# Kernel optimization log

Hardware: AMD Instinct MI355X
Metric: run time of the kernel (lower is better)

## Reference

```python
import jax, jax.numpy as jnp
import numpy as np

B, S, H, A, O = 512, 64, 1024, 1024, 1024
ATT = 64  # attention logit width (== encoder seq len)


def setup_inputs() -> dict:
    key = jax.random.key(0)
    ks = jax.random.split(key, 14)
    s = lambda *sh: 1.0 / np.sqrt(sh[-1])
    return {
        "encoder_outputs": jax.random.normal(ks[0], (B, S, A), jnp.float32),
        "hidden": jax.random.normal(ks[1], (1, B, H), jnp.float32),
        "max_length": 128,
        # attention: Linear(H+O -> 64)
        "Wa": jax.random.normal(ks[2], (ATT, H + O), jnp.float32) * s(H + O),
        "ba": jnp.zeros((ATT,), jnp.float32),
        # attention_combine: Linear(A+O -> H)
        "Wc": jax.random.normal(ks[3], (H, A + O), jnp.float32) * s(A + O),
        "bc": jnp.zeros((H,), jnp.float32),
        # GRU (1 layer): weight_ih [3H,H], weight_hh [3H,H]
        "W_ih": jax.random.normal(ks[4], (3 * H, H), jnp.float32) * s(H),
        "W_hh": jax.random.normal(ks[5], (3 * H, H), jnp.float32) * s(H),
        "b_ih": jnp.zeros((3 * H,), jnp.float32),
        "b_hh": jnp.zeros((3 * H,), jnp.float32),
        # fc_out: Linear(H -> O)
        "Wo": jax.random.normal(ks[6], (O, H), jnp.float32) * s(H),
        "bo": jnp.zeros((O,), jnp.float32),
    }


def _decode(encoder_outputs, h0, max_length, Wa, ba, Wc, bc, W_ih, W_hh, b_ih, b_hh, Wo, bo):
    Hs = h0.shape[-1]
    dec0 = jnp.zeros((encoder_outputs.shape[0], Wo.shape[0]), encoder_outputs.dtype)

    def step(carry, _):
        dec_in, h = carry  # [B,O], [B,H]
        temp = jnp.concatenate([dec_in, h], axis=1)  # [B, O+H]... matches cat(dec, hidden[-1])
        attn_w = jax.nn.softmax(temp @ Wa.T + ba, axis=1)  # [B,64]
        attn_applied = jnp.einsum("bs,bsd->bd", attn_w, encoder_outputs)  # [B,A]
        gru_in = jax.nn.relu(jnp.concatenate([dec_in, attn_applied], axis=1) @ Wc.T + bc)  # [B,H]
        # single-step PyTorch GRU cell
        gi = gru_in @ W_ih.T + b_ih  # [B,3H]
        gh = h @ W_hh.T + b_hh
        r = jax.nn.sigmoid(gi[:, :Hs] + gh[:, :Hs])
        z = jax.nn.sigmoid(gi[:, Hs:2 * Hs] + gh[:, Hs:2 * Hs])
        n = jnp.tanh(gi[:, 2 * Hs:] + r * gh[:, 2 * Hs:])
        h_new = (1.0 - z) * n + z * h
        out_tok = h_new @ Wo.T + bo  # [B,O]
        return (out_tok, h_new), out_tok

    (_, h_fin), outs = jax.lax.scan(step, (dec0, h0[0]), None, length=max_length)
    output_seq = jnp.transpose(outs, (1, 0, 2))  # [B,T,O]
    return output_seq, h_fin[None]


def reference(encoder_outputs, hidden, max_length, Wa, ba, Wc, bc, W_ih, W_hh, b_ih, b_hh, Wo, bo):
    return _decode(encoder_outputs, hidden, max_length, Wa, ba, Wc, bc, W_ih, W_hh, b_ih, b_hh, Wo, bo)
```

## Files before the change

kernel.cpp:

```cpp
#include <hip/hip_runtime.h>
#include <hip/hip_bf16.h>

#define B 512
#define S 64
#define H 1024
#define O 1024
#define T 128
#define ATT 64

typedef __bf16 bf16;
typedef __bf16 bf16x8 __attribute__((ext_vector_type(8)));
typedef __bf16 bf16x4 __attribute__((ext_vector_type(4)));
typedef float f32x4 __attribute__((ext_vector_type(4)));

static __device__ __forceinline__ float bf2f(bf16 b) {
    unsigned short s = __builtin_bit_cast(unsigned short, b);
    unsigned int u = ((unsigned int)s) << 16;
    return __builtin_bit_cast(float, u);
}
static __device__ __forceinline__ bf16 f2bf(float f) {
    unsigned int u = __builtin_bit_cast(unsigned int, f);
    unsigned int r = (u + 0x7fffu + ((u >> 16) & 1u)) >> 16;
    return __builtin_bit_cast(bf16, (unsigned short)r);
}

template <bool RELU>
__global__ __launch_bounds__(256) void gemm_kernel(
    const bf16* __restrict__ A0, const bf16* __restrict__ A1, int splitK,
    const bf16* __restrict__ W, const float* __restrict__ bias, int K,
    float* __restrict__ Cf, long ldc, bf16* __restrict__ Cbf, int ldcbf) {
    const int tid = threadIdx.x;
    const int wave = tid >> 6, lane = tid & 63;
    const int wm = wave >> 1, wn = wave & 1;
    const int quad = lane >> 4, r = lane & 15;
    const int kq = quad * 8;

    const int m0 = blockIdx.y * 32 + wm * 16 + r;
    const int n0 = blockIdx.x * 64 + wn * 32;

    const int lda0 = splitK, lda1 = K - splitK;
    const bf16* a0row = A0 + (long)m0 * lda0;
    const bf16* a1row = A1 + (long)m0 * lda1;
    const bf16* w0 = W + (long)(n0 + r) * K;
    const bf16* w1 = W + (long)(n0 + 16 + r) * K;

    f32x4 acc0 = {0.f, 0.f, 0.f, 0.f}, acc1 = {0.f, 0.f, 0.f, 0.f};

    for (int k0 = 0; k0 < K; k0 += 32) {
        bf16x8 av;
        if (k0 < splitK)
            av = *(const bf16x8*)(a0row + k0 + kq);
        else
            av = *(const bf16x8*)(a1row + (k0 - splitK) + kq);
        bf16x8 bv0 = *(const bf16x8*)(w0 + k0 + kq);
        bf16x8 bv1 = *(const bf16x8*)(w1 + k0 + kq);
        acc0 = __builtin_amdgcn_mfma_f32_16x16x32_bf16(av, bv0, acc0, 0, 0, 0);
        acc1 = __builtin_amdgcn_mfma_f32_16x16x32_bf16(av, bv1, acc1, 0, 0, 0);
    }

    const int mbase = blockIdx.y * 32 + wm * 16 + quad * 4;
    const int nA = n0 + r, nB = n0 + 16 + r;
    const float biasA = bias[nA], biasB = bias[nB];
#pragma unroll
    for (int reg = 0; reg < 4; ++reg) {
        const int m = mbase + reg;
        float vA = acc0[reg] + biasA;
        float vB = acc1[reg] + biasB;
        if (RELU) { vA = fmaxf(vA, 0.f); vB = fmaxf(vB, 0.f); }
        if (Cf) {
            Cf[(long)m * ldc + nA] = vA;
            Cf[(long)m * ldc + nB] = vB;
        }
        if (Cbf) {
            Cbf[(long)m * ldcbf + nA] = f2bf(vA);
            Cbf[(long)m * ldcbf + nB] = f2bf(vB);
        }
    }
}

__global__ __launch_bounds__(256) void attn_logits_kernel(
    const bf16* __restrict__ dec, const bf16* __restrict__ h,
    const bf16* __restrict__ Wa, const float* __restrict__ ba,
    bf16* __restrict__ attn_w) {
    __shared__ float lg[32][64];
    const int tid = threadIdx.x;
    const int wave = tid >> 6, lane = tid & 63;
    const int wm = wave >> 1, wn = wave & 1;
    const int quad = lane >> 4, r = lane & 15;
    const int kq = quad * 8;

    const int m0 = blockIdx.y * 32 + wm * 16 + r;
    const int n0 = wn * 32;

    const bf16* drow = dec + (long)m0 * H;
    const bf16* hrow = h + (long)m0 * H;
    const bf16* w0 = Wa + (long)(n0 + r) * 2048;
    const bf16* w1 = Wa + (long)(n0 + 16 + r) * 2048;

    f32x4 acc0 = {0.f, 0.f, 0.f, 0.f}, acc1 = {0.f, 0.f, 0.f, 0.f};
    for (int k0 = 0; k0 < 2048; k0 += 32) {
        bf16x8 av;
        if (k0 < 1024)
            av = *(const bf16x8*)(drow + k0 + kq);
        else
            av = *(const bf16x8*)(hrow + (k0 - 1024) + kq);
        bf16x8 bv0 = *(const bf16x8*)(w0 + k0 + kq);
        bf16x8 bv1 = *(const bf16x8*)(w1 + k0 + kq);
        acc0 = __builtin_amdgcn_mfma_f32_16x16x32_bf16(av, bv0, acc0, 0, 0, 0);
        acc1 = __builtin_amdgcn_mfma_f32_16x16x32_bf16(av, bv1, acc1, 0, 0, 0);
    }

    const int mloc = wm * 16 + quad * 4;
#pragma unroll
    for (int reg = 0; reg < 4; ++reg) {
        lg[mloc + reg][n0 + r] = acc0[reg] + ba[n0 + r];
        lg[mloc + reg][n0 + 16 + r] = acc1[reg] + ba[n0 + 16 + r];
    }
    __syncthreads();

    if (tid < 32) {
        const int row = tid;
        float mx = -1e30f;
#pragma unroll
        for (int s = 0; s < 64; ++s) mx = fmaxf(mx, lg[row][s]);
        float sum = 0.f;
#pragma unroll
        for (int s = 0; s < 64; ++s) sum += __expf(lg[row][s] - mx);
        const float inv = 1.f / sum;
        const long gb = (long)(blockIdx.y * 32 + row) * 64;
#pragma unroll
        for (int s = 0; s < 64; ++s)
            attn_w[gb + s] = f2bf(__expf(lg[row][s] - mx) * inv);
    }
}

__global__ __launch_bounds__(256) void attn_apply_kernel(
    const bf16* __restrict__ attn_w, const bf16* __restrict__ enc,
    bf16* __restrict__ attn_out) {
    __shared__ float w[64];
    const int b = blockIdx.x >> 2;
    const int d = ((blockIdx.x & 3) << 8) + threadIdx.x;
    if (threadIdx.x < 64) w[threadIdx.x] = bf2f(attn_w[b * 64 + threadIdx.x]);
    __syncthreads();
    const bf16* e = enc + (long)b * (S * 1024) + d;
    float acc = 0.f;
#pragma unroll 8
    for (int s = 0; s < S; ++s) acc += w[s] * bf2f(e[(long)s * 1024]);
    attn_out[(long)b * 1024 + d] = f2bf(acc);
}

__global__ __launch_bounds__(256) void gru_kernel(
    const bf16* __restrict__ gin, const bf16* __restrict__ hbf,
    const bf16* __restrict__ Wih, const bf16* __restrict__ Whh,
    const float* __restrict__ bih, const float* __restrict__ bhh,
    const float* __restrict__ hold, float* __restrict__ hnew,
    bf16* __restrict__ hnewbf) {
    const int tid = threadIdx.x;
    const int wave = tid >> 6, lane = tid & 63;
    const int wm = wave >> 1, wn = wave & 1;
    const int quad = lane >> 4, r = lane & 15;
    const int kq = quad * 8;

    const int m0 = blockIdx.y * 32 + wm * 16 + r;
    const int n0 = blockIdx.x * 64 + wn * 32;

    const bf16* grow = gin + (long)m0 * H;
    const bf16* hrow = hbf + (long)m0 * H;

    const bf16* wi[3][2];
    const bf16* wh[3][2];
#pragma unroll
    for (int g = 0; g < 3; ++g) {
#pragma unroll
        for (int ni = 0; ni < 2; ++ni) {
            const long row = (long)g * H + n0 + ni * 16 + r;
            wi[g][ni] = Wih + row * H;
            wh[g][ni] = Whh + row * H;
        }
    }

    f32x4 aI[3][2], aH[3][2];
#pragma unroll
    for (int g = 0; g < 3; ++g)
#pragma unroll
        for (int ni = 0; ni < 2; ++ni) {
            aI[g][ni] = (f32x4){0.f, 0.f, 0.f, 0.f};
            aH[g][ni] = (f32x4){0.f, 0.f, 0.f, 0.f};
        }

    for (int k0 = 0; k0 < H; k0 += 32) {
        const int ko = k0 + kq;
        bf16x8 ai = *(const bf16x8*)(grow + ko);
        bf16x8 ah = *(const bf16x8*)(hrow + ko);
#pragma unroll
        for (int g = 0; g < 3; ++g) {
#pragma unroll
            for (int ni = 0; ni < 2; ++ni) {
                bf16x8 bi = *(const bf16x8*)(wi[g][ni] + ko);
                aI[g][ni] = __builtin_amdgcn_mfma_f32_16x16x32_bf16(ai, bi, aI[g][ni], 0, 0, 0);
                bf16x8 bh = *(const bf16x8*)(wh[g][ni] + ko);
                aH[g][ni] = __builtin_amdgcn_mfma_f32_16x16x32_bf16(ah, bh, aH[g][ni], 0, 0, 0);
            }
        }
    }

    const int mbase = blockIdx.y * 32 + wm * 16 + quad * 4;
#pragma unroll
    for (int ni = 0; ni < 2; ++ni) {
        const int j = n0 + ni * 16 + r;
        const float bir = bih[j], biz = bih[j + H], bin = bih[j + 2 * H];
        const float bhr = bhh[j], bhz = bhh[j + H], bhn = bhh[j + 2 * H];
#pragma unroll
        for (int reg = 0; reg < 4; ++reg) {
            const int m = mbase + reg;
            const float gir = aI[0][ni][reg] + bir, ghr = aH[0][ni][reg] + bhr;
            const float giz = aI[1][ni][reg] + biz, ghz = aH[1][ni][reg] + bhz;
            const float ginv = aI[2][ni][reg] + bin, ghn = aH[2][ni][reg] + bhn;
            const float rg = 1.f / (1.f + __expf(-(gir + ghr)));
            const float zg = 1.f / (1.f + __expf(-(giz + ghz)));
            const float ng = tanhf(ginv + rg * ghn);
            const long idx = (long)m * H + j;
            const float hv = hold[idx];
            const float hnv = (1.f - zg) * ng + zg * hv;
            hnew[idx] = hnv;
            hnewbf[idx] = f2bf(hnv);
        }
    }
}

__global__ __launch_bounds__(256) void cast_kernel(
    const float* __restrict__ src, bf16* __restrict__ dst, long n4) {
    long i = (long)blockIdx.x * blockDim.x + threadIdx.x;
    const long stride = (long)gridDim.x * blockDim.x;
    for (; i < n4; i += stride) {
        float4 v = ((const float4*)src)[i];
        bf16x4 o = {f2bf(v.x), f2bf(v.y), f2bf(v.z), f2bf(v.w)};
        *(bf16x4*)(dst + 4 * i) = o;
    }
}

__global__ __launch_bounds__(256) void init_h_kernel(
    const float* __restrict__ h0, float* __restrict__ hfp,
    bf16* __restrict__ hbf, long n4) {
    long i = (long)blockIdx.x * blockDim.x + threadIdx.x;
    const long stride = (long)gridDim.x * blockDim.x;
    for (; i < n4; i += stride) {
        float4 v = ((const float4*)h0)[i];
        ((float4*)hfp)[i] = v;
        bf16x4 o = {f2bf(v.x), f2bf(v.y), f2bf(v.z), f2bf(v.w)};
        *(bf16x4*)(hbf + 4 * i) = o;
    }
}

__global__ __launch_bounds__(256) void copy_f32_kernel(
    const float* __restrict__ src, float* __restrict__ dst, long n4) {
    long i = (long)blockIdx.x * blockDim.x + threadIdx.x;
    const long stride = (long)gridDim.x * blockDim.x;
    for (; i < n4; i += stride) ((float4*)dst)[i] = ((const float4*)src)[i];
}

extern "C" void kernel_launch(void* const* d_in, const int* in_sizes, int n_in,
                              void* d_out, int out_size, void* d_ws, size_t ws_size,
                              hipStream_t stream) {
    const float* enc_f = (const float*)d_in[0];
    const float* hidden = (const float*)d_in[1];
    const float* Wa = (const float*)d_in[3];
    const float* ba = (const float*)d_in[4];
    const float* Wc = (const float*)d_in[5];
    const float* bc = (const float*)d_in[6];
    const float* Wih = (const float*)d_in[7];
    const float* Whh = (const float*)d_in[8];
    const float* bih = (const float*)d_in[9];
    const float* bhh = (const float*)d_in[10];
    const float* Wo = (const float*)d_in[11];
    const float* bo = (const float*)d_in[12];
    float* out = (float*)d_out;

    char* p = (char*)d_ws;
    auto carve = [&](long bytes) {
        char* q = p;
        p += (bytes + 255) & ~255L;
        return q;
    };
    bf16* Wa_bf  = (bf16*)carve((long)ATT * 2048 * 2);
    bf16* Wc_bf  = (bf16*)carve((long)H * 2048 * 2);
    bf16* Wih_bf = (bf16*)carve((long)3 * H * H * 2);
    bf16* Whh_bf = (bf16*)carve((long)3 * H * H * 2);
    bf16* Wo_bf  = (bf16*)carve((long)O * H * 2);
    bf16* enc_bf = (bf16*)carve((long)B * S * 1024 * 2);
    bf16* dec_bf = (bf16*)carve((long)B * O * 2);
    bf16* attn_bf = (bf16*)carve((long)B * 1024 * 2);
    bf16* gru_bf = (bf16*)carve((long)B * H * 2);
    bf16* hbfA = (bf16*)carve((long)B * H * 2);
    bf16* hbfB = (bf16*)carve((long)B * H * 2);
    bf16* attn_w = (bf16*)carve((long)B * 64 * 2);
    float* hfpA = (float*)carve((long)B * H * 4);
    float* hfpB = (float*)carve((long)B * H * 4);

    hipMemsetAsync(dec_bf, 0, (long)B * O * 2, stream);
    auto cast = [&](const float* s, bf16* d, long n) {
        long n4 = n / 4;
        int blocks = (int)((n4 + 255) / 256);
        if (blocks > 4096) blocks = 4096;
        cast_kernel<<<blocks, 256, 0, stream>>>(s, d, n4);
    };
    cast(Wa, Wa_bf, (long)ATT * 2048);
    cast(Wc, Wc_bf, (long)H * 2048);
    cast(Wih, Wih_bf, (long)3 * H * H);
    cast(Whh, Whh_bf, (long)3 * H * H);
    cast(Wo, Wo_bf, (long)O * H);
    cast(enc_f, enc_bf, (long)B * S * 1024);
    init_h_kernel<<<512, 256, 0, stream>>>(hidden, hfpA, hbfA, (long)B * H / 4);

    const dim3 blk(256);
    const dim3 grid_gemm(H / 64, B / 32);
    const dim3 grid_attn(1, B / 32);

    for (int t = 0; t < T; ++t) {
        const bf16* hbf_r = (t & 1) ? hbfB : hbfA;
        bf16* hbf_w = (t & 1) ? hbfA : hbfB;
        const float* hfp_r = (t & 1) ? hfpB : hfpA;
        float* hfp_w = (t & 1) ? hfpA : hfpB;

        attn_logits_kernel<<<grid_attn, blk, 0, stream>>>(dec_bf, hbf_r, Wa_bf, ba, attn_w);
        attn_apply_kernel<<<B * 4, blk, 0, stream>>>(attn_w, enc_bf, attn_bf);
        gemm_kernel<true><<<grid_gemm, blk, 0, stream>>>(
            dec_bf, attn_bf, 1024, Wc_bf, bc, 2048, nullptr, 0, gru_bf, H);
        gru_kernel<<<grid_gemm, blk, 0, stream>>>(
            gru_bf, hbf_r, Wih_bf, Whh_bf, bih, bhh, hfp_r, hfp_w, hbf_w);
        gemm_kernel<false><<<grid_gemm, blk, 0, stream>>>(
            hbf_w, hbf_w, 1024, Wo_bf, bo, 1024,
            out + (long)t * O, (long)T * O, dec_bf, O);
    }

    copy_f32_kernel<<<512, 256, 0, stream>>>(hfpA, out + (long)B * T * O, (long)B * H / 4);
}
```

Baseline: 17.34 ms.

## Fold output projection into attention/combine weights and batch fc_out after recurrence

Since dec_in equals h_prev·Wo^T+bo, the output projection is folded algebraically into the attention-logit and combine weights (Wa_eff = Wa_dec·Wo + Wa_h, Wd = Wc_dec·Wo, with folded biases), precomputed once by an fp32 sgemm. This removes the per-step fc_out GEMM and the dec-input K half from the critical recurrence. All hidden states are stored so fc_out runs as one large batched GEMM at the end. Attention-apply is vectorized to 4 elements per thread. Precomputing products in fp32 and then rounding to bf16 changes numerics slightly. The path also needs extra workspace for all T hidden states and falls back to per-step fc_out if that space is missing.

```diff
diff --git a/kernel.cpp b/kernel.cpp
--- a/kernel.cpp
+++ b/kernel.cpp
@@ -24,11 +24,82 @@
     return __builtin_bit_cast(bf16, (unsigned short)r);
 }
 
-template <bool RELU>
-__global__ __launch_bounds__(256) void gemm_kernel(
-    const bf16* __restrict__ A0, const bf16* __restrict__ A1, int splitK,
-    const bf16* __restrict__ W, const float* __restrict__ bias, int K,
-    float* __restrict__ Cf, long ldc, bf16* __restrict__ Cbf, int ldcbf) {
+__global__ __launch_bounds__(128) void attn_logits_kernel(
+    const bf16* __restrict__ h, const bf16* __restrict__ W, int ldw,
+    const float* __restrict__ bias, bf16* __restrict__ attn_w) {
+    __shared__ float lg[16][64];
+    const int tid = threadIdx.x;
+    const int wn = tid >> 6, lane = tid & 63;
+    const int quad = lane >> 4, r = lane & 15;
+    const int kq = quad * 8;
+
+    const int m0 = blockIdx.y * 16 + r;
+    const int n0 = wn * 32;
+
+    const bf16* hrow = h + (long)m0 * H + kq;
+    const bf16* w0 = W + (long)(n0 + r) * ldw + kq;
+    const bf16* w1 = W + (long)(n0 + 16 + r) * ldw + kq;
+
+    f32x4 acc0 = {0.f, 0.f, 0.f, 0.f}, acc1 = {0.f, 0.f, 0.f, 0.f};
+#pragma unroll 4
+    for (int k = 0; k < H; k += 32) {
+        bf16x8 av = *(const bf16x8*)(hrow + k);
+        bf16x8 b0 = *(const bf16x8*)(w0 + k);
+        bf16x8 b1 = *(const bf16x8*)(w1 + k);
+        acc0 = __builtin_amdgcn_mfma_f32_16x16x32_bf16(av, b0, acc0, 0, 0, 0);
+        acc1 = __builtin_amdgcn_mfma_f32_16x16x32_bf16(av, b1, acc1, 0, 0, 0);
+    }
+
+    const int mloc = quad * 4;
+#pragma unroll
+    for (int reg = 0; reg < 4; ++reg) {
+        lg[mloc + reg][n0 + r] = acc0[reg] + bias[n0 + r];
+        lg[mloc + reg][n0 + 16 + r] = acc1[reg] + bias[n0 + 16 + r];
+    }
+    __syncthreads();
+
+    if (tid < 16) {
+        const int row = tid;
+        float mx = -1e30f;
+#pragma unroll
+        for (int s = 0; s < 64; ++s) mx = fmaxf(mx, lg[row][s]);
+        float sum = 0.f;
+#pragma unroll
+        for (int s = 0; s < 64; ++s) sum += __expf(lg[row][s] - mx);
+        const float inv = 1.f / sum;
+        const long gb = (long)(blockIdx.y * 16 + row) * 64;
+#pragma unroll
+        for (int s = 0; s < 64; ++s)
+            attn_w[gb + s] = f2bf(__expf(lg[row][s] - mx) * inv);
+    }
+}
+
+__global__ __launch_bounds__(256) void attn_apply_kernel(
+    const bf16* __restrict__ attn_w, const bf16* __restrict__ enc,
+    bf16* __restrict__ attn_out) {
+    __shared__ float w[64];
+    const int b = blockIdx.x;
+    const int t = threadIdx.x;
+    if (t < 64) w[t] = bf2f(attn_w[b * 64 + t]);
+    __syncthreads();
+    const bf16* e = enc + (long)b * (S * 1024) + 4 * t;
+    float a0 = 0.f, a1 = 0.f, a2 = 0.f, a3 = 0.f;
+#pragma unroll 8
+    for (int s = 0; s < S; ++s) {
+        bf16x4 v = *(const bf16x4*)(e + (long)s * 1024);
+        const float ws = w[s];
+        a0 += ws * bf2f(v[0]); a1 += ws * bf2f(v[1]);
+        a2 += ws * bf2f(v[2]); a3 += ws * bf2f(v[3]);
+    }
+    bf16x4 o = {f2bf(a0), f2bf(a1), f2bf(a2), f2bf(a3)};
+    *(bf16x4*)(attn_out + (long)b * 1024 + 4 * t) = o;
+}
+
+template <int K0>
+__global__ __launch_bounds__(256) void combine_kernel(
+    const bf16* __restrict__ A0, const bf16* __restrict__ W0,
+    const bf16* __restrict__ A1, const bf16* __restrict__ W1, int ldw1,
+    const float* __restrict__ bias, bf16* __restrict__ Cout) {
     const int tid = threadIdx.x;
     const int wave = tid >> 6, lane = tid & 63;
     const int wm = wave >> 1, wn = wave & 1;
@@ -38,24 +109,33 @@
     const int m0 = blockIdx.y * 32 + wm * 16 + r;
     const int n0 = blockIdx.x * 64 + wn * 32;
 
-    const int lda0 = splitK, lda1 = K - splitK;
-    const bf16* a0row = A0 + (long)m0 * lda0;
-    const bf16* a1row = A1 + (long)m0 * lda1;
-    const bf16* w0 = W + (long)(n0 + r) * K;
-    const bf16* w1 = W + (long)(n0 + 16 + r) * K;
-
     f32x4 acc0 = {0.f, 0.f, 0.f, 0.f}, acc1 = {0.f, 0.f, 0.f, 0.f};
 
-    for (int k0 = 0; k0 < K; k0 += 32) {
-        bf16x8 av;
-        if (k0 < splitK)
-            av = *(const bf16x8*)(a0row + k0 + kq);
-        else
-            av = *(const bf16x8*)(a1row + (k0 - splitK) + kq);
-        bf16x8 bv0 = *(const bf16x8*)(w0 + k0 + kq);
-        bf16x8 bv1 = *(const bf16x8*)(w1 + k0 + kq);
-        acc0 = __builtin_amdgcn_mfma_f32_16x16x32_bf16(av, bv0, acc0, 0, 0, 0);
-        acc1 = __builtin_amdgcn_mfma_f32_16x16x32_bf16(av, bv1, acc1, 0, 0, 0);
+    if (K0 > 0) {
+        const bf16* a = A0 + (long)m0 * H + kq;
+        const bf16* w0 = W0 + (long)(n0 + r) * H + kq;
+        const bf16* w1 = W0 + (long)(n0 + 16 + r) * H + kq;
+#pragma unroll 4
+        for (int k = 0; k < K0; k += 32) {
+            bf16x8 av = *(const bf16x8*)(a + k);
+            bf16x8 b0 = *(const bf16x8*)(w0 + k);
+            bf16x8 b1 = *(const bf16x8*)(w1 + k);
+            acc0 = __builtin_amdgcn_mfma_f32_16x16x32_bf16(av, b0, acc0, 0, 0, 0);
+            acc1 = __builtin_amdgcn_mfma_f32_16x16x32_bf16(av, b1, acc1, 0, 0, 0);
+        }
+    }
+    {
+        const bf16* a = A1 + (long)m0 * H + kq;
+        const bf16* w0 = W1 + (long)(n0 + r) * ldw1 + kq;
+        const bf16* w1 = W1 + (long)(n0 + 16 + r) * ldw1 + kq;
+#pragma unroll 4
+        for (int k = 0; k < H; k += 32) {
+            bf16x8 av = *(const bf16x8*)(a + k);
+            bf16x8 b0 = *(const bf16x8*)(w0 + k);
+            bf16x8 b1 = *(const bf16x8*)(w1 + k);
+            acc0 = __builtin_amdgcn_mfma_f32_16x16x32_bf16(av, b0, acc0, 0, 0, 0);
+            acc1 = __builtin_amdgcn_mfma_f32_16x16x32_bf16(av, b1, acc1, 0, 0, 0);
+        }
     }
 
     const int mbase = blockIdx.y * 32 + wm * 16 + quad * 4;
@@ -64,25 +144,15 @@
 #pragma unroll
     for (int reg = 0; reg < 4; ++reg) {
         const int m = mbase + reg;
-        float vA = acc0[reg] + biasA;
-        float vB = acc1[reg] + biasB;
-        if (RELU) { vA = fmaxf(vA, 0.f); vB = fmaxf(vB, 0.f); }
-        if (Cf) {
-            Cf[(long)m * ldc + nA] = vA;
-            Cf[(long)m * ldc + nB] = vB;
-        }
-        if (Cbf) {
-            Cbf[(long)m * ldcbf + nA] = f2bf(vA);
-            Cbf[(long)m * ldcbf + nB] = f2bf(vB);
-        }
-    }
-}
-
-__global__ __launch_bounds__(256) void attn_logits_kernel(
-    const bf16* __restrict__ dec, const bf16* __restrict__ h,
-    const bf16* __restrict__ Wa, const float* __restrict__ ba,
-    bf16* __restrict__ attn_w) {
-    __shared__ float lg[32][64];
+        Cout[(long)m * H + nA] = f2bf(fmaxf(acc0[reg] + biasA, 0.f));
+        Cout[(long)m * H + nB] = f2bf(fmaxf(acc1[reg] + biasB, 0.f));
+    }
+}
+
+template <bool REMAP>
+__global__ __launch_bounds__(256) void fc_kernel(
+    const bf16* __restrict__ A, const bf16* __restrict__ W,
+    const float* __restrict__ bias, float* __restrict__ out, long ldc) {
     const int tid = threadIdx.x;
     const int wave = tid >> 6, lane = tid & 63;
     const int wm = wave >> 1, wn = wave & 1;
@@ -90,63 +160,36 @@
     const int kq = quad * 8;
 
     const int m0 = blockIdx.y * 32 + wm * 16 + r;
-    const int n0 = wn * 32;
-
-    const bf16* drow = dec + (long)m0 * H;
-    const bf16* hrow = h + (long)m0 * H;
-    const bf16* w0 = Wa + (long)(n0 + r) * 2048;
-    const bf16* w1 = Wa + (long)(n0 + 16 + r) * 2048;
+    const int n0 = blockIdx.x * 64 + wn * 32;
+
+    const bf16* a = A + (long)m0 * H + kq;
+    const bf16* w0 = W + (long)(n0 + r) * H + kq;
+    const bf16* w1 = W + (long)(n0 + 16 + r) * H + kq;
 
     f32x4 acc0 = {0.f, 0.f, 0.f, 0.f}, acc1 = {0.f, 0.f, 0.f, 0.f};
-    for (int k0 = 0; k0 < 2048; k0 += 32) {
-        bf16x8 av;
-        if (k0 < 1024)
-            av = *(const bf16x8*)(drow + k0 + kq);
+#pragma unroll 4
+    for (int k = 0; k < H; k += 32) {
+        bf16x8 av = *(const bf16x8*)(a + k);
+        bf16x8 b0 = *(const bf16x8*)(w0 + k);
+        bf16x8 b1 = *(const bf16x8*)(w1 + k);
+        acc0 = __builtin_amdgcn_mfma_f32_16x16x32_bf16(av, b0, acc0, 0, 0, 0);
+        acc1 = __builtin_amdgcn_mfma_f32_16x16x32_bf16(av, b1, acc1, 0, 0, 0);
+    }
+
+    const int mbase = blockIdx.y * 32 + wm * 16 + quad * 4;
+    const int nA = n0 + r, nB = n0 + 16 + r;
+    const float biasA = bias[nA], biasB = bias[nB];
+#pragma unroll
+    for (int reg = 0; reg < 4; ++reg) {
+        const int m = mbase + reg;
+        long base;
+        if (REMAP)
+            base = (long)(m & (B - 1)) * ((long)T * O) + (long)(m >> 9) * O;
         else
-            av = *(const bf16x8*)(hrow + (k0 - 1024) + kq);
-        bf16x8 bv0 = *(const bf16x8*)(w0 + k0 + kq);
-        bf16x8 bv1 = *(const bf16x8*)(w1 + k0 + kq);
-        acc0 = __builtin_amdgcn_mfma_f32_16x16x32_bf16(av, bv0, acc0, 0, 0, 0);
-        acc1 = __builtin_amdgcn_mfma_f32_16x16x32_bf16(av, bv1, acc1, 0, 0, 0);
-    }
-
-    const int mloc = wm * 16 + quad * 4;
-#pragma unroll
-    for (int reg = 0; reg < 4; ++reg) {
-        lg[mloc + reg][n0 + r] = acc0[reg] + ba[n0 + r];
-        lg[mloc + reg][n0 + 16 + r] = acc1[reg] + ba[n0 + 16 + r];
-    }
-    __syncthreads();
-
-    if (tid < 32) {
-        const int row = tid;
-        float mx = -1e30f;
-#pragma unroll
-        for (int s = 0; s < 64; ++s) mx = fmaxf(mx, lg[row][s]);
-        float sum = 0.f;
-#pragma unroll
-        for (int s = 0; s < 64; ++s) sum += __expf(lg[row][s] - mx);
-        const float inv = 1.f / sum;
-        const long gb = (long)(blockIdx.y * 32 + row) * 64;
-#pragma unroll
-        for (int s = 0; s < 64; ++s)
-            attn_w[gb + s] = f2bf(__expf(lg[row][s] - mx) * inv);
-    }
-}
-
-__global__ __launch_bounds__(256) void attn_apply_kernel(
-    const bf16* __restrict__ attn_w, const bf16* __restrict__ enc,
-    bf16* __restrict__ attn_out) {
-    __shared__ float w[64];
-    const int b = blockIdx.x >> 2;
-    const int d = ((blockIdx.x & 3) << 8) + threadIdx.x;
-    if (threadIdx.x < 64) w[threadIdx.x] = bf2f(attn_w[b * 64 + threadIdx.x]);
-    __syncthreads();
-    const bf16* e = enc + (long)b * (S * 1024) + d;
-    float acc = 0.f;
-#pragma unroll 8
-    for (int s = 0; s < S; ++s) acc += w[s] * bf2f(e[(long)s * 1024]);
-    attn_out[(long)b * 1024 + d] = f2bf(acc);
+            base = (long)m * ldc;
+        out[base + nA] = acc0[reg] + biasA;
+        out[base + nB] = acc1[reg] + biasB;
+    }
 }
 
 __global__ __launch_bounds__(256) void gru_kernel(
@@ -164,20 +207,19 @@
     const int m0 = blockIdx.y * 32 + wm * 16 + r;
     const int n0 = blockIdx.x * 64 + wn * 32;
 
-    const bf16* grow = gin + (long)m0 * H;
-    const bf16* hrow = hbf + (long)m0 * H;
+    const bf16* grow = gin + (long)m0 * H + kq;
+    const bf16* hrow = hbf + (long)m0 * H + kq;
 
     const bf16* wi[3][2];
     const bf16* wh[3][2];
 #pragma unroll
-    for (int g = 0; g < 3; ++g) {
+    for (int g = 0; g < 3; ++g)
 #pragma unroll
         for (int ni = 0; ni < 2; ++ni) {
             const long row = (long)g * H + n0 + ni * 16 + r;
-            wi[g][ni] = Wih + row * H;
-            wh[g][ni] = Whh + row * H;
-        }
-    }
+            wi[g][ni] = Wih + row * H + kq;
+            wh[g][ni] = Whh + row * H + kq;
+        }
 
     f32x4 aI[3][2], aH[3][2];
 #pragma unroll
@@ -188,20 +230,19 @@
             aH[g][ni] = (f32x4){0.f, 0.f, 0.f, 0.f};
         }
 
-    for (int k0 = 0; k0 < H; k0 += 32) {
-        const int ko = k0 + kq;
-        bf16x8 ai = *(const bf16x8*)(grow + ko);
-        bf16x8 ah = *(const bf16x8*)(hrow + ko);
-#pragma unroll
-        for (int g = 0; g < 3; ++g) {
+#pragma unroll 2
+    for (int k = 0; k < H; k += 32) {
+        bf16x8 ai = *(const bf16x8*)(grow + k);
+        bf16x8 ah = *(const bf16x8*)(hrow + k);
+#pragma unroll
+        for (int g = 0; g < 3; ++g)
 #pragma unroll
             for (int ni = 0; ni < 2; ++ni) {
-                bf16x8 bi = *(const bf16x8*)(wi[g][ni] + ko);
+                bf16x8 bi = *(const bf16x8*)(wi[g][ni] + k);
                 aI[g][ni] = __builtin_amdgcn_mfma_f32_16x16x32_bf16(ai, bi, aI[g][ni], 0, 0, 0);
-                bf16x8 bh = *(const bf16x8*)(wh[g][ni] + ko);
+                bf16x8 bh = *(const bf16x8*)(wh[g][ni] + k);
                 aH[g][ni] = __builtin_amdgcn_mfma_f32_16x16x32_bf16(ah, bh, aH[g][ni], 0, 0, 0);
             }
-        }
     }
 
     const int mbase = blockIdx.y * 32 + wm * 16 + quad * 4;
@@ -226,6 +267,55 @@
             hnewbf[idx] = f2bf(hnv);
         }
     }
+}
+
+__global__ __launch_bounds__(256) void sgemm_bf16out(
+    const float* __restrict__ A, int lda, const float* __restrict__ Bm, int ldb,
+    const float* __restrict__ C0, int ldc0, float beta,
+    bf16* __restrict__ D, int ldd, int M, int K) {
+    __shared__ float As[32][33], Bs[32][33];
+    const int tx = threadIdx.x & 15, ty = threadIdx.x >> 4;
+    const int bx = blockIdx.x * 32, by = blockIdx.y * 32;
+    float acc[2][2] = {{0.f, 0.f}, {0.f, 0.f}};
+    for (int k0 = 0; k0 < K; k0 += 32) {
+        for (int i = threadIdx.x; i < 1024; i += 256) {
+            const int rr = i >> 5, cc = i & 31;
+            const int gr = by + rr;
+            As[rr][cc] = (gr < M) ? A[(long)gr * lda + k0 + cc] : 0.f;
+            Bs[rr][cc] = Bm[(long)(k0 + rr) * ldb + bx + cc];
+        }
+        __syncthreads();
+#pragma unroll
+        for (int kk = 0; kk < 32; ++kk) {
+            const float a0 = As[ty * 2][kk], a1 = As[ty * 2 + 1][kk];
+            const float b0 = Bs[kk][tx * 2], b1 = Bs[kk][tx * 2 + 1];
+            acc[0][0] += a0 * b0; acc[0][1] += a0 * b1;
+            acc[1][0] += a1 * b0; acc[1][1] += a1 * b1;
+        }
+        __syncthreads();
+    }
+#pragma unroll
+    for (int i = 0; i < 2; ++i)
+#pragma unroll
+        for (int j = 0; j < 2; ++j) {
+            const int gr = by + ty * 2 + i, gc = bx + tx * 2 + j;
+            if (gr < M) {
+                float v = acc[i][j];
+                if (C0) v += beta * C0[(long)gr * ldc0 + gc];
+                D[(long)gr * ldd + gc] = f2bf(v);
+            }
+        }
+}
+
+__global__ __launch_bounds__(256) void bias_dot_kernel(
+    const float* __restrict__ Wsrc, int ld, const float* __restrict__ bsrc,
+    const float* __restrict__ bo, float* __restrict__ dst, int n) {
+    const int j = blockIdx.x * 256 + threadIdx.x;
+    if (j >= n) return;
+    float s = bsrc[j];
+    const float* row = Wsrc + (long)j * ld;
+    for (int m = 0; m < 1024; ++m) s += row[m] * bo[m];
+    dst[j] = s;
 }
 
 __global__ __launch_bounds__(256) void cast_kernel(
@@ -282,22 +372,33 @@
         p += (bytes + 255) & ~255L;
         return q;
     };
-    bf16* Wa_bf  = (bf16*)carve((long)ATT * 2048 * 2);
-    bf16* Wc_bf  = (bf16*)carve((long)H * 2048 * 2);
-    bf16* Wih_bf = (bf16*)carve((long)3 * H * H * 2);
-    bf16* Whh_bf = (bf16*)carve((long)3 * H * H * 2);
-    bf16* Wo_bf  = (bf16*)carve((long)O * H * 2);
-    bf16* enc_bf = (bf16*)carve((long)B * S * 1024 * 2);
-    bf16* dec_bf = (bf16*)carve((long)B * O * 2);
+    bf16* Wa_bf   = (bf16*)carve((long)ATT * 2048 * 2);
+    bf16* Wc_bf   = (bf16*)carve((long)H * 2048 * 2);
+    bf16* Wih_bf  = (bf16*)carve((long)3 * H * H * 2);
+    bf16* Whh_bf  = (bf16*)carve((long)3 * H * H * 2);
+    bf16* Wo_bf   = (bf16*)carve((long)O * H * 2);
+    bf16* Wd_bf   = (bf16*)carve((long)H * H * 2);
+    bf16* Waeff_bf = (bf16*)carve((long)ATT * H * 2);
+    bf16* enc_bf  = (bf16*)carve((long)B * S * 1024 * 2);
+    bf16* attn_w  = (bf16*)carve((long)B * 64 * 2);
     bf16* attn_bf = (bf16*)carve((long)B * 1024 * 2);
-    bf16* gru_bf = (bf16*)carve((long)B * H * 2);
-    bf16* hbfA = (bf16*)carve((long)B * H * 2);
-    bf16* hbfB = (bf16*)carve((long)B * H * 2);
-    bf16* attn_w = (bf16*)carve((long)B * 64 * 2);
-    float* hfpA = (float*)carve((long)B * H * 4);
-    float* hfpB = (float*)carve((long)B * H * 4);
-
-    hipMemsetAsync(dec_bf, 0, (long)B * O * 2, stream);
+    bf16* gru_bf  = (bf16*)carve((long)B * H * 2);
+    float* hfpA   = (float*)carve((long)B * H * 4);
+    float* hfpB   = (float*)carve((long)B * H * 4);
+    float* ba_eff = (float*)carve((long)ATT * 4);
+    float* bc_eff = (float*)carve((long)H * 4);
+
+    const long hall_bytes = (long)(T + 1) * B * H * 2;
+    const long used = (long)(p - (char*)d_ws);
+    const bool hall = ((long)ws_size - used) >= (hall_bytes + 4096);
+    bf16* Hall = nullptr; bf16* hbfA = nullptr; bf16* hbfB = nullptr;
+    if (hall) {
+        Hall = (bf16*)carve(hall_bytes);
+    } else {
+        hbfA = (bf16*)carve((long)B * H * 2);
+        hbfB = (bf16*)carve((long)B * H * 2);
+    }
+
     auto cast = [&](const float* s, bf16* d, long n) {
         long n4 = n / 4;
         int blocks = (int)((n4 + 255) / 256);
@@ -310,28 +411,56 @@
     cast(Whh, Whh_bf, (long)3 * H * H);
     cast(Wo, Wo_bf, (long)O * H);
     cast(enc_f, enc_bf, (long)B * S * 1024);
-    init_h_kernel<<<512, 256, 0, stream>>>(hidden, hfpA, hbfA, (long)B * H / 4);
+    init_h_kernel<<<512, 256, 0, stream>>>(hidden, hfpA,
+                                           hall ? Hall : hbfA, (long)B * H / 4);
+
+    sgemm_bf16out<<<dim3(32, 32), 256, 0, stream>>>(
+        Wc, 2048, Wo, 1024, nullptr, 0, 0.f, Wd_bf, 1024, 1024, 1024);
+    sgemm_bf16out<<<dim3(32, 2), 256, 0, stream>>>(
+        Wa, 2048, Wo, 1024, Wa + 1024, 2048, 1.f, Waeff_bf, 1024, 64, 1024);
+    bias_dot_kernel<<<4, 256, 0, stream>>>(Wc, 2048, bc, bo, bc_eff, 1024);
+    bias_dot_kernel<<<1, 256, 0, stream>>>(Wa, 2048, ba, bo, ba_eff, 64);
 
     const dim3 blk(256);
     const dim3 grid_gemm(H / 64, B / 32);
-    const dim3 grid_attn(1, B / 32);
+    const dim3 grid_lg(1, B / 16);
 
     for (int t = 0; t < T; ++t) {
-        const bf16* hbf_r = (t & 1) ? hbfB : hbfA;
-        bf16* hbf_w = (t & 1) ? hbfA : hbfB;
+        const bf16* hbf_r = hall ? (Hall + (long)t * B * H)
+                                 : ((t & 1) ? hbfB : hbfA);
+        bf16* hbf_w = hall ? (Hall + (long)(t + 1) * B * H)
+                           : ((t & 1) ? hbfA : hbfB);
         const float* hfp_r = (t & 1) ? hfpB : hfpA;
         float* hfp_w = (t & 1) ? hfpA : hfpB;
 
-        attn_logits_kernel<<<grid_attn, blk, 0, stream>>>(dec_bf, hbf_r, Wa_bf, ba, attn_w);
-        attn_apply_kernel<<<B * 4, blk, 0, stream>>>(attn_w, enc_bf, attn_bf);
-        gemm_kernel<true><<<grid_gemm, blk, 0, stream>>>(
-            dec_bf, attn_bf, 1024, Wc_bf, bc, 2048, nullptr, 0, gru_bf, H);
+        if (t == 0)
+            attn_logits_kernel<<<grid_lg, 128, 0, stream>>>(
+                hbf_r, Wa_bf + 1024, 2048, ba, attn_w);
+        else
+            attn_logits_kernel<<<grid_lg, 128, 0, stream>>>(
+                hbf_r, Waeff_bf, 1024, ba_eff, attn_w);
+
+        attn_apply_kernel<<<B, blk, 0, stream>>>(attn_w, enc_bf, attn_bf);
+
+        if (t == 0)
+            combine_kernel<0><<<grid_gemm, blk, 0, stream>>>(
+                hbf_r, Wd_bf, attn_bf, Wc_bf + 1024, 2048, bc, gru_bf);
+        else
+            combine_kernel<1024><<<grid_gemm, blk, 0, stream>>>(
+                hbf_r, Wd_bf, attn_bf, Wc_bf + 1024, 2048, bc_eff, gru_bf);
+
         gru_kernel<<<grid_gemm, blk, 0, stream>>>(
             gru_bf, hbf_r, Wih_bf, Whh_bf, bih, bhh, hfp_r, hfp_w, hbf_w);
-        gemm_kernel<false><<<grid_gemm, blk, 0, stream>>>(
-            hbf_w, hbf_w, 1024, Wo_bf, bo, 1024,
-            out + (long)t * O, (long)T * O, dec_bf, O);
-    }
-
-    copy_f32_kernel<<<512, 256, 0, stream>>>(hfpA, out + (long)B * T * O, (long)B * H / 4);
-}
+
+        if (!hall)
+            fc_kernel<false><<<grid_gemm, blk, 0, stream>>>(
+                hbf_w, Wo_bf, bo, out + (long)t * O, (long)T * O);
+    }
+
+    if (hall)
+        fc_kernel<true><<<dim3(O / 64, (T * B) / 32), blk, 0, stream>>>(
+            Hall + (long)B * H, Wo_bf, bo, out, 0);
+
+    copy_f32_kernel<<<512, 256, 0, stream>>>(hfpA, out + (long)B * T * O,
+                                             (long)B * H / 4);
+}
```

Result: slower. 19.55 ms (+12.7%).
